# Optimization experiments

Hardware: AMD Instinct MI355X
Metric: run time of the kernel (lower is better)

Reference implementation:

```python
import jax, jax.numpy as jnp
import numpy as np

IN_FEATURES = 4096
OUT_FEATURES = 4096
KERNEL_SIZE = 4  # MaxPool1d stride defaults to kernel_size
SCALE = 0.5


def setup_inputs() -> dict:
    key = jax.random.key(0)
    kx, kw, kb = jax.random.split(key, 3)
    bound = 1.0 / np.sqrt(IN_FEATURES)
    x = jax.random.normal(kx, (4096, IN_FEATURES), dtype=jnp.float32)
    W = jax.random.uniform(kw, (OUT_FEATURES, IN_FEATURES), dtype=jnp.float32, minval=-bound, maxval=bound)
    b = jax.random.uniform(kb, (OUT_FEATURES,), dtype=jnp.float32, minval=-bound, maxval=bound)
    return {"x": x, "W": W, "b": b}


def reference(x, W, b) -> jnp.ndarray:
    # Linear: [B, I] @ [I, O] + [O] -> [B, O]
    y = jnp.einsum("bi,oi->bo", x, W) + b
    B, O = y.shape
    K = KERNEL_SIZE
    n_win = (O - K) // K + 1  # stride == kernel_size, no padding
    # Non-overlapping window max-pool: [B, n_win, K] -> max over K
    pooled = y[:, : n_win * K].reshape(B, n_win, K).max(axis=-1)
    # Sum over pooled dim, then scale -> [B]
    return pooled.sum(axis=-1) * SCALE
```

## Files before the change

### kernel.cpp

```cpp
#include <hip/hip_runtime.h>
#include <hip/hip_bf16.h>

#define KDIM 4096
#define NTILE 64
#define NELEM16 (1u << 24)

typedef float f32x4 __attribute__((ext_vector_type(4)));
typedef short bf16x8 __attribute__((ext_vector_type(8)));

__device__ __forceinline__ unsigned int pack_bf16x2(float lo, float hi) {
    __hip_bfloat162 h = __float22bfloat162_rn(float2{lo, hi});
    union { __hip_bfloat162 h; unsigned int u; } c; c.h = h; return c.u;
}

__global__ __launch_bounds__(256)
void pack_frag2(const float* __restrict__ x, const float* __restrict__ W,
                unsigned short* __restrict__ xb, unsigned short* __restrict__ wb)
{
    const unsigned int stride = gridDim.x * blockDim.x;
    for (unsigned int i = blockIdx.x * blockDim.x + threadIdx.x; i < (1u << 22); i += stride) {
        const unsigned int j  = i & ((1u << 21) - 1);
        const float* __restrict__ in = (i >> 21) ? W : x;
        unsigned short* __restrict__ out = (i >> 21) ? wb : xb;
        const unsigned int lane = j & 63;
        const unsigned int s    = (j >> 6) & 1;
        const unsigned int f    = (j >> 7) & 15;
        const unsigned int kt   = (j >> 11) & 63;
        const unsigned int t    = j >> 17;
        const unsigned int row  = t * 256 + f * 16 + (lane & 15);
        const unsigned int col  = kt * 64 + s * 32 + (lane >> 4) * 8;
        const float4* sp = (const float4*)(in + (size_t)row * KDIM + col);
        const float4 a = sp[0], b = sp[1];
        uint4 o;
        o.x = pack_bf16x2(a.x, a.y); o.y = pack_bf16x2(a.z, a.w);
        o.z = pack_bf16x2(b.x, b.y); o.w = pack_bf16x2(b.z, b.w);
        *(uint4*)(out + (size_t)j * 8) = o;
    }
}

#define LOADS(AB, BB, t, s)                                                     \
    _Pragma("unroll") for (int m = 0; m < 8; ++m)                               \
        AB[m] = *(const bf16x8*)&Ab[(size_t)(t) * 16384 +                       \
            (((m * 2 + wm) * 2 + (s)) * 512) + lane * 8];                       \
    _Pragma("unroll") for (int n = 0; n < 4; ++n)                               \
        BB[n] = *(const bf16x8*)&Bb[(size_t)(t) * 16384 +                       \
            (((n * 4 + wn) * 2 + (s)) * 512) + lane * 8];

#define MFMAH(AB, BB)                                                           \
    __builtin_amdgcn_s_setprio(1);                                              \
    _Pragma("unroll") for (int m = 0; m < 8; ++m)                               \
      _Pragma("unroll") for (int n = 0; n < 4; ++n)                             \
        acc[m][n] = __builtin_amdgcn_mfma_f32_16x16x32_bf16(                    \
            AB[m], BB[n], acc[m][n], 0, 0, 0);                                  \
    __builtin_amdgcn_s_setprio(0);

__global__ __launch_bounds__(512, 1)
void gemm_nolds(const unsigned short* __restrict__ A,
                const unsigned short* __restrict__ B,
                const float* __restrict__ bias,
                float* __restrict__ out)
{
    const int tid  = threadIdx.x;
    const int lane = tid & 63;
    const int wid  = tid >> 6;
    const int wm   = wid >> 2;
    const int wn   = wid & 3;
    const int c15  = lane & 15;
    const int q4   = lane >> 4;

    const int bid = blockIdx.x;
    const int wg  = (bid & 7) * 32 + (bid >> 3);
    const int bm  = wg >> 4;
    const int bn  = wg & 15;

    const unsigned short* Ab = A + ((size_t)bm << 20);
    const unsigned short* Bb = B + ((size_t)bn << 20);

    f32x4 acc[8][4];
    #pragma unroll
    for (int i = 0; i < 8; ++i)
        #pragma unroll
        for (int j = 0; j < 4; ++j)
            acc[i][j] = (f32x4)0.0f;

    bf16x8 aX[8], bX[4];
    bf16x8 aY[8], bY[4];

    LOADS(aX, bX, 0, 0);

    for (int t = 0; t < NTILE; ++t) {
        LOADS(aY, bY, t, 1);
        MFMAH(aX, bX);
        if (t + 1 < NTILE) { LOADS(aX, bX, t + 1, 0); }
        MFMAH(aY, bY);
    }

    float rs[8][4];
    #pragma unroll
    for (int mf = 0; mf < 8; ++mf)
        #pragma unroll
        for (int r = 0; r < 4; ++r)
            rs[mf][r] = 0.0f;

    #pragma unroll
    for (int nf = 0; nf < 4; ++nf) {
        const float bv = bias[bn * 256 + (nf * 4 + wn) * 16 + c15];
        #pragma unroll
        for (int mf = 0; mf < 8; ++mf) {
            #pragma unroll
            for (int r = 0; r < 4; ++r) {
                float v = acc[mf][nf][r] + bv;
                v = fmaxf(v, __shfl_xor(v, 1));
                v = fmaxf(v, __shfl_xor(v, 2));
                v += __shfl_xor(v, 4);
                v += __shfl_xor(v, 8);
                rs[mf][r] += v;
            }
        }
    }

    if (c15 == 0) {
        #pragma unroll
        for (int mf = 0; mf < 8; ++mf)
            #pragma unroll
            for (int r = 0; r < 4; ++r) {
                const int row = bm * 256 + (mf * 2 + wm) * 16 + q4 * 4 + r;
                atomicAdd(&out[row], 0.5f * rs[mf][r]);
            }
    }
}

__global__ __launch_bounds__(256, 2)
void fused_gemm_pool_fallback(const float* __restrict__ x,
                              const float* __restrict__ W,
                              const float* __restrict__ b,
                              float* __restrict__ out)
{
    __shared__ unsigned short As[128][72];
    __shared__ unsigned short Bs[128][72];

    const int tid  = threadIdx.x;
    const int lane = tid & 63;
    const int wid  = tid >> 6;
    const int wm   = wid >> 1;
    const int wn   = wid & 1;

    const int bid = blockIdx.x;
    const int wg  = (bid & 7) * 128 + (bid >> 3);
    const int bm  = wg >> 5;
    const int bn  = wg & 31;

    const int srow = tid >> 4;
    const int scol = tid & 15;

    const float* xbase = x + (size_t)(bm * 128 + srow) * KDIM + scol * 4;
    const float* wbase = W + (size_t)(bn * 128 + srow) * KDIM + scol * 4;

    f32x4 acc[4][4];
    #pragma unroll
    for (int i = 0; i < 4; ++i)
        #pragma unroll
        for (int j = 0; j < 4; ++j)
            acc[i][j] = (f32x4)0.0f;

    float4 ra[8], rb[8];
    #pragma unroll
    for (int p = 0; p < 8; ++p) {
        ra[p] = *(const float4*)(xbase + (size_t)(p * 16) * KDIM);
        rb[p] = *(const float4*)(wbase + (size_t)(p * 16) * KDIM);
    }

    for (int kt = 0; kt < KDIM / 64; ++kt) {
        #pragma unroll
        for (int p = 0; p < 8; ++p) {
            const int r = srow + p * 16;
            uint2 pa, pb;
            pa.x = pack_bf16x2(ra[p].x, ra[p].y);
            pa.y = pack_bf16x2(ra[p].z, ra[p].w);
            pb.x = pack_bf16x2(rb[p].x, rb[p].y);
            pb.y = pack_bf16x2(rb[p].z, rb[p].w);
            *(uint2*)&As[r][scol * 4] = pa;
            *(uint2*)&Bs[r][scol * 4] = pb;
        }
        __syncthreads();

        if (kt + 1 < KDIM / 64) {
            const float* xa = xbase + (size_t)(kt + 1) * 64;
            const float* wa = wbase + (size_t)(kt + 1) * 64;
            #pragma unroll
            for (int p = 0; p < 8; ++p) {
                ra[p] = *(const float4*)(xa + (size_t)(p * 16) * KDIM);
                rb[p] = *(const float4*)(wa + (size_t)(p * 16) * KDIM);
            }
        }

        #pragma unroll
        for (int k0 = 0; k0 < 2; ++k0) {
            const int kk = k0 * 32 + (lane >> 4) * 8;
            bf16x8 af[4], bfr[4];
            #pragma unroll
            for (int mf = 0; mf < 4; ++mf)
                af[mf] = *(const bf16x8*)&As[wm * 64 + mf * 16 + (lane & 15)][kk];
            #pragma unroll
            for (int nf = 0; nf < 4; ++nf)
                bfr[nf] = *(const bf16x8*)&Bs[wn * 64 + nf * 16 + (lane & 15)][kk];
            #pragma unroll
            for (int mf = 0; mf < 4; ++mf)
                #pragma unroll
                for (int nf = 0; nf < 4; ++nf)
                    acc[mf][nf] = __builtin_amdgcn_mfma_f32_16x16x32_bf16(
                        af[mf], bfr[nf], acc[mf][nf], 0, 0, 0);
        }
        __syncthreads();
    }

    float rs[4][4];
    #pragma unroll
    for (int mf = 0; mf < 4; ++mf)
        #pragma unroll
        for (int r = 0; r < 4; ++r)
            rs[mf][r] = 0.0f;

    #pragma unroll
    for (int nf = 0; nf < 4; ++nf) {
        const float bv = b[bn * 128 + wn * 64 + nf * 16 + (lane & 15)];
        #pragma unroll
        for (int mf = 0; mf < 4; ++mf) {
            #pragma unroll
            for (int r = 0; r < 4; ++r) {
                float v = acc[mf][nf][r] + bv;
                v = fmaxf(v, __shfl_xor(v, 1));
                v = fmaxf(v, __shfl_xor(v, 2));
                v += __shfl_xor(v, 4);
                v += __shfl_xor(v, 8);
                rs[mf][r] += v;
            }
        }
    }

    if ((lane & 15) == 0) {
        #pragma unroll
        for (int mf = 0; mf < 4; ++mf)
            #pragma unroll
            for (int r = 0; r < 4; ++r) {
                const int row = bm * 128 + wm * 64 + mf * 16 + (lane >> 4) * 4 + r;
                atomicAdd(&out[row], 0.5f * rs[mf][r]);
            }
    }
}

extern "C" void kernel_launch(void* const* d_in, const int* in_sizes, int n_in,
                              void* d_out, int out_size, void* d_ws, size_t ws_size,
                              hipStream_t stream) {
    const float* x = (const float*)d_in[0];
    const float* W = (const float*)d_in[1];
    const float* b = (const float*)d_in[2];
    float* out = (float*)d_out;

    hipMemsetAsync(out, 0, (size_t)out_size * sizeof(float), stream);

    const size_t need = (size_t)NELEM16 * 2 * sizeof(unsigned short);
    if (ws_size >= need) {
        unsigned short* xb = (unsigned short*)d_ws;
        unsigned short* wb = xb + (size_t)NELEM16;
        pack_frag2<<<dim3(2048), dim3(256), 0, stream>>>(x, W, xb, wb);
        gemm_nolds<<<dim3(256), dim3(512), 0, stream>>>(xb, wb, b, out);
    } else {
        fused_gemm_pool_fallback<<<dim3(1024), dim3(256), 0, stream>>>(x, W, b, out);
    }
}
```

Before: 184.8 us.

## Stage tiles through LDS with direct global-to-LDS loads and triple buffering

Replaces the register-only GEMM, which loaded MFMA fragments straight from global memory, with a kernel that streams pre-swizzled bf16 tiles into LDS using global_load_lds. It uses a three-stage buffer with explicit vmcnt waits and barriers. The block tile shrinks from 256x256 to 256x128 with 512 blocks, and the pack kernel writes an XOR-swizzled layout to avoid LDS bank conflicts. This is meant to cut global-load latency stalls and improve overlap, at the cost of barrier synchronisation, more blocks and atomics, and lower per-block data reuse.

```diff
diff --git a/kernel.cpp b/kernel.cpp
--- a/kernel.cpp
+++ b/kernel.cpp
@@ -2,11 +2,18 @@
 #include <hip/hip_bf16.h>
 
 #define KDIM 4096
-#define NTILE 64
+#define NKT 128
 #define NELEM16 (1u << 24)
 
 typedef float f32x4 __attribute__((ext_vector_type(4)));
 typedef short bf16x8 __attribute__((ext_vector_type(8)));
+
+typedef const __attribute__((address_space(1))) unsigned int g_u32;
+typedef __attribute__((address_space(3))) unsigned int l_u32;
+
+__device__ __forceinline__ void gload_lds16(const void* g, void* l) {
+    __builtin_amdgcn_global_load_lds((g_u32*)g, (l_u32*)l, 16, 0, 0);
+}
 
 __device__ __forceinline__ unsigned int pack_bf16x2(float lo, float hi) {
     __hip_bfloat162 h = __float22bfloat162_rn(float2{lo, hi});
@@ -14,21 +21,33 @@
 }
 
 __global__ __launch_bounds__(256)
-void pack_frag2(const float* __restrict__ x, const float* __restrict__ W,
-                unsigned short* __restrict__ xb, unsigned short* __restrict__ wb)
+void pack3(const float* __restrict__ x, const float* __restrict__ W,
+           unsigned short* __restrict__ xb, unsigned short* __restrict__ wb)
 {
     const unsigned int stride = gridDim.x * blockDim.x;
     for (unsigned int i = blockIdx.x * blockDim.x + threadIdx.x; i < (1u << 22); i += stride) {
-        const unsigned int j  = i & ((1u << 21) - 1);
-        const float* __restrict__ in = (i >> 21) ? W : x;
-        unsigned short* __restrict__ out = (i >> 21) ? wb : xb;
-        const unsigned int lane = j & 63;
-        const unsigned int s    = (j >> 6) & 1;
-        const unsigned int f    = (j >> 7) & 15;
-        const unsigned int kt   = (j >> 11) & 63;
-        const unsigned int t    = j >> 17;
-        const unsigned int row  = t * 256 + f * 16 + (lane & 15);
-        const unsigned int col  = kt * 64 + s * 32 + (lane >> 4) * 8;
+        const float* __restrict__ in;
+        unsigned short* __restrict__ out;
+        unsigned int row, col, j;
+        if (i < (1u << 21)) {
+            j = i;
+            const unsigned int cp = j & 3;
+            const unsigned int rl = (j >> 2) & 255;
+            const unsigned int kt = (j >> 10) & 127;
+            const unsigned int mt = j >> 17;
+            row = mt * 256 + rl;
+            col = kt * 32 + (cp ^ (rl & 3)) * 8;
+            in = x; out = xb;
+        } else {
+            j = i - (1u << 21);
+            const unsigned int cp = j & 3;
+            const unsigned int rl = (j >> 2) & 127;
+            const unsigned int kt = (j >> 9) & 127;
+            const unsigned int nt = j >> 16;
+            row = nt * 128 + rl;
+            col = kt * 32 + (cp ^ (rl & 3)) * 8;
+            in = W; out = wb;
+        }
         const float4* sp = (const float4*)(in + (size_t)row * KDIM + col);
         const float4 a = sp[0], b = sp[1];
         uint4 o;
@@ -38,75 +57,106 @@
     }
 }
 
-#define LOADS(AB, BB, t, s)                                                     \
-    _Pragma("unroll") for (int m = 0; m < 8; ++m)                               \
-        AB[m] = *(const bf16x8*)&Ab[(size_t)(t) * 16384 +                       \
-            (((m * 2 + wm) * 2 + (s)) * 512) + lane * 8];                       \
-    _Pragma("unroll") for (int n = 0; n < 4; ++n)                               \
-        BB[n] = *(const bf16x8*)&Bb[(size_t)(t) * 16384 +                       \
-            (((n * 4 + wn) * 2 + (s)) * 512) + lane * 8];
-
-#define MFMAH(AB, BB)                                                           \
+#define STAGE3(kt, BUFE)                                                        \
+    {                                                                           \
+        const unsigned short* ga = Abase + (size_t)(kt) * 8192 + wid * 1024 + lane * 8; \
+        gload_lds16(ga,       &lds[(BUFE) + wid * 1024]);                       \
+        gload_lds16(ga + 512, &lds[(BUFE) + wid * 1024 + 512]);                 \
+        const unsigned short* gb = Bbase + (size_t)(kt) * 4096 + wid * 512 + lane * 8;  \
+        gload_lds16(gb,       &lds[(BUFE) + 8192 + wid * 512]);                 \
+    }
+
+#define READ_AB(BUFE)                                                           \
+    _Pragma("unroll") for (int mf = 0; mf < 4; ++mf)                            \
+        afr[mf] = *(const bf16x8*)&lds[(BUFE) + rdA + mf * 512];                \
+    _Pragma("unroll") for (int nf = 0; nf < 4; ++nf)                            \
+        bfr[nf] = *(const bf16x8*)&lds[(BUFE) + rdB + nf * 512];
+
+#define MFMA16()                                                                \
     __builtin_amdgcn_s_setprio(1);                                              \
-    _Pragma("unroll") for (int m = 0; m < 8; ++m)                               \
-      _Pragma("unroll") for (int n = 0; n < 4; ++n)                             \
-        acc[m][n] = __builtin_amdgcn_mfma_f32_16x16x32_bf16(                    \
-            AB[m], BB[n], acc[m][n], 0, 0, 0);                                  \
+    _Pragma("unroll") for (int mf = 0; mf < 4; ++mf)                            \
+      _Pragma("unroll") for (int nf = 0; nf < 4; ++nf)                          \
+        acc[mf][nf] = __builtin_amdgcn_mfma_f32_16x16x32_bf16(                  \
+            afr[mf], bfr[nf], acc[mf][nf], 0, 0, 0);                            \
     __builtin_amdgcn_s_setprio(0);
 
-__global__ __launch_bounds__(512, 1)
-void gemm_nolds(const unsigned short* __restrict__ A,
+#define PHASE(t, BUFE, STGE, VMW)                                               \
+    {                                                                           \
+        READ_AB(BUFE);                                                          \
+        MFMA16();                                                               \
+        if ((t) + 2 < NKT) STAGE3((t) + 2, STGE);                               \
+        VMW;                                                                    \
+        __builtin_amdgcn_s_barrier();                                           \
+        __builtin_amdgcn_sched_barrier(0);                                      \
+    }
+
+#define VM3 asm volatile("s_waitcnt vmcnt(3)" ::: "memory")
+#define VM0 asm volatile("s_waitcnt vmcnt(0)" ::: "memory")
+
+__global__ __launch_bounds__(512, 4)
+void gemm_cores(const unsigned short* __restrict__ A,
                 const unsigned short* __restrict__ B,
                 const float* __restrict__ bias,
                 float* __restrict__ out)
 {
+    __shared__ unsigned short lds[36864];
+
     const int tid  = threadIdx.x;
     const int lane = tid & 63;
     const int wid  = tid >> 6;
-    const int wm   = wid >> 2;
-    const int wn   = wid & 3;
+    const int wm   = wid >> 1;
+    const int wn   = wid & 1;
     const int c15  = lane & 15;
     const int q4   = lane >> 4;
 
     const int bid = blockIdx.x;
-    const int wg  = (bid & 7) * 32 + (bid >> 3);
-    const int bm  = wg >> 4;
-    const int bn  = wg & 15;
-
-    const unsigned short* Ab = A + ((size_t)bm << 20);
-    const unsigned short* Bb = B + ((size_t)bn << 20);
-
-    f32x4 acc[8][4];
-    #pragma unroll
-    for (int i = 0; i < 8; ++i)
+    const int wg  = (bid & 7) * 64 + (bid >> 3);
+    const int bm  = wg >> 5;
+    const int bn  = wg & 31;
+
+    const unsigned short* Abase = A + ((size_t)bm << 20);
+    const unsigned short* Bbase = B + ((size_t)bn << 19);
+
+    const int swz = ((q4 ^ (c15 & 3)) * 8);
+    const int rdA = (wm * 64 + c15) * 32 + swz;
+    const int rdB = 8192 + (wn * 64 + c15) * 32 + swz;
+
+    f32x4 acc[4][4];
+    #pragma unroll
+    for (int i = 0; i < 4; ++i)
         #pragma unroll
         for (int j = 0; j < 4; ++j)
             acc[i][j] = (f32x4)0.0f;
 
-    bf16x8 aX[8], bX[4];
-    bf16x8 aY[8], bY[4];
-
-    LOADS(aX, bX, 0, 0);
-
-    for (int t = 0; t < NTILE; ++t) {
-        LOADS(aY, bY, t, 1);
-        MFMAH(aX, bX);
-        if (t + 1 < NTILE) { LOADS(aX, bX, t + 1, 0); }
-        MFMAH(aY, bY);
-    }
-
-    float rs[8][4];
-    #pragma unroll
-    for (int mf = 0; mf < 8; ++mf)
+    bf16x8 afr[4], bfr[4];
+
+    STAGE3(0, 0);
+    STAGE3(1, 12288);
+    VM3;
+    __builtin_amdgcn_s_barrier();
+    __builtin_amdgcn_sched_barrier(0);
+
+    for (int tt = 0; tt < 126; tt += 3) {
+        PHASE(tt,     0,     24576, VM3);
+        PHASE(tt + 1, 12288, 0,     VM3);
+        PHASE(tt + 2, 24576, 12288, VM3);
+    }
+    PHASE(126, 0, 24576, VM0);
+    READ_AB(12288);
+    MFMA16();
+
+    float rs[4][4];
+    #pragma unroll
+    for (int mf = 0; mf < 4; ++mf)
         #pragma unroll
         for (int r = 0; r < 4; ++r)
             rs[mf][r] = 0.0f;
 
     #pragma unroll
     for (int nf = 0; nf < 4; ++nf) {
-        const float bv = bias[bn * 256 + (nf * 4 + wn) * 16 + c15];
-        #pragma unroll
-        for (int mf = 0; mf < 8; ++mf) {
+        const float bv = bias[bn * 128 + wn * 64 + nf * 16 + c15];
+        #pragma unroll
+        for (int mf = 0; mf < 4; ++mf) {
             #pragma unroll
             for (int r = 0; r < 4; ++r) {
                 float v = acc[mf][nf][r] + bv;
@@ -121,10 +171,10 @@
 
     if (c15 == 0) {
         #pragma unroll
-        for (int mf = 0; mf < 8; ++mf)
+        for (int mf = 0; mf < 4; ++mf)
             #pragma unroll
             for (int r = 0; r < 4; ++r) {
-                const int row = bm * 256 + (mf * 2 + wm) * 16 + q4 * 4 + r;
+                const int row = bm * 256 + wm * 64 + mf * 16 + q4 * 4 + r;
                 atomicAdd(&out[row], 0.5f * rs[mf][r]);
             }
     }
@@ -263,8 +313,8 @@
     if (ws_size >= need) {
         unsigned short* xb = (unsigned short*)d_ws;
         unsigned short* wb = xb + (size_t)NELEM16;
-        pack_frag2<<<dim3(2048), dim3(256), 0, stream>>>(x, W, xb, wb);
-        gemm_nolds<<<dim3(256), dim3(512), 0, stream>>>(xb, wb, b, out);
+        pack3<<<dim3(2048), dim3(256), 0, stream>>>(x, W, xb, wb);
+        gemm_cores<<<dim3(512), dim3(512), 0, stream>>>(xb, wb, b, out);
     } else {
         fused_gemm_pool_fallback<<<dim3(1024), dim3(256), 0, stream>>>(x, W, b, out);
     }
```

Result: faster. 175.3 us (-5.2%).
